# Optimization experiments

Hardware: AMD Instinct MI355X
Metric: run time of the kernel (lower is better)

Reference implementation:

```python
import jax, jax.numpy as jnp
import numpy as np

N = 100000
E = 1600000
F_NODE = 6
F_EDGE = 2
H = 64


def _glorot(key, shape):
    lim = float(np.sqrt(6.0 / (shape[0] + shape[1])))
    return jax.random.uniform(key, shape, jnp.float32, -lim, lim)


def setup_inputs() -> dict:
    key = jax.random.key(0)
    ks = jax.random.split(key, 16)
    inp = {
        "x": jax.random.normal(ks[0], (N, F_NODE), jnp.float32),
        "edge_index": jax.random.randint(ks[1], (2, E), 0, N, jnp.int64),
        "edge_attr": jax.random.normal(ks[2], (E, F_EDGE), jnp.float32),
        # GCN layers (PyG GCNConv: linear no-bias, then aggregate, then +bias)
        "W1": _glorot(ks[3], (F_NODE, H)), "b1": jnp.zeros((H,), jnp.float32),
        "W2": _glorot(ks[4], (H, H)), "b2": jnp.zeros((H,), jnp.float32),
        "W3": _glorot(ks[5], (H, H)), "b3": jnp.zeros((H,), jnp.float32),
        # edge_mlp
        "We1": _glorot(ks[6], (F_EDGE, H)), "be1": jnp.zeros((H,), jnp.float32),
        "We2": _glorot(ks[7], (H, H)), "be2": jnp.zeros((H,), jnp.float32),
        # predictor
        "Wp1": _glorot(ks[8], (3 * H, H)), "bp1": jnp.zeros((H,), jnp.float32),
        "Wp2": _glorot(ks[9], (H, H // 2)), "bp2": jnp.zeros((H // 2,), jnp.float32),
        "Wp3": _glorot(ks[10], (H // 2, 1)), "bp3": jnp.zeros((1,), jnp.float32),
    }
    return inp


def _gcn_conv(h, W, b, src_sl, dst_sl, norm, n):
    # PyG GCNConv with self-loops and symmetric normalization
    h = h @ W                                   # [N, H_out]
    msg = h[src_sl] * norm[:, None]             # gather + scale per edge(+loop)
    out = jax.ops.segment_sum(msg, dst_sl, num_segments=n)
    return out + b


def _forward(x, edge_attr, W1, b1, W2, b2, W3, b3, We1, be1, We2, be2,
             Wp1, bp1, Wp2, bp2, Wp3, bp3, edge_index):
    n = x.shape[0]
    src, dst = edge_index[0], edge_index[1]

    # --- edge feature injection (vectorized version of per-edge loop) ---
    ef = jax.nn.relu(edge_attr @ We1 + be1) @ We2 + be2      # [E, H]
    nef = (jax.ops.segment_sum(ef, src, num_segments=n)
           + jax.ops.segment_sum(ef, dst, num_segments=n))   # [N, H]
    ones_e = jnp.ones((ef.shape[0],), x.dtype)
    deg = (jax.ops.segment_sum(ones_e, src, num_segments=n)
           + jax.ops.segment_sum(ones_e, dst, num_segments=n))
    deg = jnp.maximum(deg, 1.0)
    nef = nef / deg[:, None]
    # hidden_dim (64) >= node feature dim (6) -> truncate
    x = x + nef[:, : x.shape[1]] * 0.5

    # --- GCN normalization with self-loops (shared across layers) ---
    loop = jnp.arange(n, dtype=src.dtype)
    src_sl = jnp.concatenate([src, loop])
    dst_sl = jnp.concatenate([dst, loop])
    deg_sl = jax.ops.segment_sum(jnp.ones_like(dst_sl, dtype=x.dtype), dst_sl,
                                 num_segments=n)
    dinv = jnp.where(deg_sl > 0, deg_sl ** -0.5, 0.0)
    norm = dinv[src_sl] * dinv[dst_sl]

    h = jax.nn.relu(_gcn_conv(x, W1, b1, src_sl, dst_sl, norm, n))
    h = jax.nn.relu(_gcn_conv(h, W2, b2, src_sl, dst_sl, norm, n))
    h = _gcn_conv(h, W3, b3, src_sl, dst_sl, norm, n)

    graph_emb = h.mean(axis=0)                 # global_mean_pool, batch=None
    node_mean = h.mean(axis=0)
    node_std = jnp.std(h, axis=0, ddof=1)      # torch.std is unbiased
    combined = jnp.concatenate([graph_emb, node_mean, node_std])  # [3H]

    p = jax.nn.relu(combined @ Wp1 + bp1)      # dropout inactive in eval
    p = jax.nn.relu(p @ Wp2 + bp2)
    out = jax.nn.sigmoid(p @ Wp3 + bp3)        # (1,)
    return out


def reference(x, edge_index, edge_attr, W1, b1, W2, b2, W3, b3,
              We1, be1, We2, be2, Wp1, bp1, Wp2, bp2, Wp3, bp3):
    return _forward(x, edge_attr, W1, b1, W2, b2, W3, b3, We1, be1, We2, be2,
                    Wp1, bp1, Wp2, bp2, Wp3, bp3, edge_index)
```

## Files before the change

### kernel.cpp

```cpp
#include <hip/hip_runtime.h>
#include <hip/hip_bf16.h>
#include <stdint.h>

typedef float floatx2 __attribute__((ext_vector_type(2)));
typedef unsigned uint32x4 __attribute__((ext_vector_type(4)));

__device__ __forceinline__ float rdlane(float v, int l) {
    return __uint_as_float(__builtin_amdgcn_readlane(__float_as_uint(v), l));
}
__device__ __forceinline__ unsigned pk_fp8x4(float a, float b, float c, float d) {
    int u = __builtin_amdgcn_cvt_pk_fp8_f32(a, b, 0, false);
    u = __builtin_amdgcn_cvt_pk_fp8_f32(c, d, u, true);
    return (unsigned)u;
}
__device__ __forceinline__ unsigned pk_fp8x2(float a, float b) {
    return (unsigned)__builtin_amdgcn_cvt_pk_fp8_f32(a, b, 0, false);
}

__global__ void k_zero(int* __restrict__ cntO, int* __restrict__ cntI,
                       double* __restrict__ sums, int n) {
    int i = blockIdx.x * blockDim.x + threadIdx.x;
    if (i < 128) sums[i] = 0.0;
    if (i < n) { cntO[i] = 0; cntI[i] = 0; }
}

__global__ __launch_bounds__(256) void k_front(
    const int* __restrict__ ei, const float* __restrict__ ea,
    const float* __restrict__ We1, const float* __restrict__ be1,
    const float* __restrict__ We2, const float* __restrict__ be2,
    uint2* __restrict__ efp, int* __restrict__ cntO, int* __restrict__ cntI,
    int* __restrict__ rankS, int* __restrict__ rankD, int E) {
    __shared__ float sWe1[128], sbe1[64], sWe2[64 * 6], sbe2[6];
    int t = threadIdx.x;
    if (t < 128) sWe1[t] = We1[t];
    if (t < 64) {
        sbe1[t] = be1[t];
#pragma unroll
        for (int c = 0; c < 6; ++c) sWe2[t * 6 + c] = We2[t * 64 + c];
    }
    if (t < 6) sbe2[t] = be2[t];
    __syncthreads();

    int e = blockIdx.x * blockDim.x + t;
    if (e >= E) return;

    int s = ei[e], d = ei[E + e];
    int rs = atomicAdd(&cntO[s], 1);
    int rd = atomicAdd(&cntI[d], 1);

    float2 aa = ((const float2*)ea)[e];
    float acc[6];
#pragma unroll
    for (int c = 0; c < 6; ++c) acc[c] = sbe2[c];
#pragma unroll
    for (int j = 0; j < 64; ++j) {
        float h = fmaf(aa.x, sWe1[j], fmaf(aa.y, sWe1[64 + j], sbe1[j]));
        h = fmaxf(h, 0.f);
#pragma unroll
        for (int c = 0; c < 6; ++c) acc[c] = fmaf(h, sWe2[j * 6 + c], acc[c]);
    }
    efp[e] = make_uint2(pk_fp8x4(acc[0], acc[1], acc[2], acc[3]),
                        pk_fp8x2(acc[4], acc[5]));
    rankS[e] = rs;
    rankD[e] = rd;
}

__global__ __launch_bounds__(256) void k_scan1(const int* __restrict__ cntO,
                                               const int* __restrict__ cntI,
                                               int2* __restrict__ bsum, int n) {
    __shared__ int2 l[256];
    int i = blockIdx.x * 256 + threadIdx.x;
    l[threadIdx.x] = (i < n) ? make_int2(cntO[i], cntI[i]) : make_int2(0, 0);
    __syncthreads();
    for (int s = 128; s > 0; s >>= 1) {
        if (threadIdx.x < s) {
            l[threadIdx.x].x += l[threadIdx.x + s].x;
            l[threadIdx.x].y += l[threadIdx.x + s].y;
        }
        __syncthreads();
    }
    if (threadIdx.x == 0) bsum[blockIdx.x] = l[0];
}
__global__ __launch_bounds__(512) void k_scan2(int2* __restrict__ bsum, int nb,
                                               int* __restrict__ offON,
                                               int* __restrict__ offIN) {
    __shared__ int2 l[512];
    int t = threadIdx.x;
    int2 v = (t < nb) ? bsum[t] : make_int2(0, 0);
    l[t] = v;
    __syncthreads();
    for (int s = 1; s < 512; s <<= 1) {
        int2 tmp = (t >= s) ? l[t - s] : make_int2(0, 0);
        __syncthreads();
        l[t].x += tmp.x; l[t].y += tmp.y;
        __syncthreads();
    }
    if (t < nb) bsum[t] = make_int2(l[t].x - v.x, l[t].y - v.y);
    if (t == 511) { *offON = l[511].x; *offIN = l[511].y; }
}
__global__ __launch_bounds__(256) void k_scan3off(const int* __restrict__ cntO,
                                                  const int* __restrict__ cntI,
                                                  const int2* __restrict__ bsum,
                                                  int* __restrict__ offO,
                                                  int* __restrict__ offI, int n) {
    __shared__ int2 l[256];
    int i = blockIdx.x * 256 + threadIdx.x;
    int2 v = (i < n) ? make_int2(cntO[i], cntI[i]) : make_int2(0, 0);
    l[threadIdx.x] = v;
    __syncthreads();
    for (int s = 1; s < 256; s <<= 1) {
        int2 tmp = (threadIdx.x >= (unsigned)s) ? l[threadIdx.x - s] : make_int2(0, 0);
        __syncthreads();
        l[threadIdx.x].x += tmp.x; l[threadIdx.x].y += tmp.y;
        __syncthreads();
    }
    if (i < n) {
        int2 bs = bsum[blockIdx.x];
        offO[i] = l[threadIdx.x].x - v.x + bs.x;
        offI[i] = l[threadIdx.x].y - v.y + bs.y;
    }
}

__global__ __launch_bounds__(256) void k_place(const int* __restrict__ ei,
                                               const int* __restrict__ rankS,
                                               const int* __restrict__ rankD,
                                               const int* __restrict__ offO,
                                               const int* __restrict__ offI,
                                               const uint2* __restrict__ efp,
                                               uint2* __restrict__ out_rec,
                                               uint4* __restrict__ in_rec, int E) {
    int e = blockIdx.x * blockDim.x + threadIdx.x;
    if (e >= E) return;
    int s = ei[e], d = ei[E + e];
    uint2 f = efp[e];
    out_rec[offO[s] + rankS[e]] = f;
    in_rec[offI[d] + rankD[e]] = make_uint4((unsigned)s, f.x, f.y, 0u);
}

__global__ __launch_bounds__(256) void k_nefmm1(
    const int* __restrict__ offO, const uint2* __restrict__ out_rec,
    const int* __restrict__ offI, const uint4* __restrict__ in_rec,
    const float* __restrict__ x, const float* __restrict__ W1,
    float* __restrict__ dinv, int* __restrict__ in_src,
    unsigned* __restrict__ sOut, int n) {
    __shared__ float sW1[384];
    int t = threadIdx.x;
    for (int idx = t; idx < 384; idx += 256) sW1[idx] = W1[idx];
    __syncthreads();

    int i = blockIdx.x * blockDim.x + t;
    if (i >= n) return;
    int bo = offO[i], eo = offO[i + 1];
    int bi = offI[i], eiN = offI[i + 1];
    float a0 = 0.f, a1 = 0.f, a2 = 0.f, a3 = 0.f, a4 = 0.f, a5 = 0.f;
    for (int j = bo; j < eo; ++j) {
        uint2 q = out_rec[j];
        floatx2 p01 = __builtin_amdgcn_cvt_pk_f32_fp8(q.x, false);
        floatx2 p23 = __builtin_amdgcn_cvt_pk_f32_fp8(q.x, true);
        floatx2 p45 = __builtin_amdgcn_cvt_pk_f32_fp8(q.y, false);
        a0 += p01.x; a1 += p01.y; a2 += p23.x;
        a3 += p23.y; a4 += p45.x; a5 += p45.y;
    }
    for (int j = bi; j < eiN; ++j) {
        uint4 r = in_rec[j];
        __builtin_nontemporal_store((int)r.x, in_src + j);
        floatx2 p01 = __builtin_amdgcn_cvt_pk_f32_fp8(r.y, false);
        floatx2 p23 = __builtin_amdgcn_cvt_pk_f32_fp8(r.y, true);
        floatx2 p45 = __builtin_amdgcn_cvt_pk_f32_fp8(r.z, false);
        a0 += p01.x; a1 += p01.y; a2 += p23.x;
        a3 += p23.y; a4 += p45.x; a5 += p45.y;
    }
    int indeg = eiN - bi;
    float degf = (float)((eo - bo) + indeg);
    float inv = 0.5f / fmaxf(degf, 1.f);
    const float2* xr = (const float2*)(x + (size_t)i * 6);
    float2 x01 = xr[0], x23 = xr[1], x45 = xr[2];
    float xp0 = x01.x + a0 * inv, xp1 = x01.y + a1 * inv;
    float xp2 = x23.x + a2 * inv, xp3 = x23.y + a3 * inv;
    float xp4 = x45.x + a4 * inv, xp5 = x45.y + a5 * inv;
    float dv = 1.f / sqrtf(1.f + (float)indeg);
    dinv[i] = dv;

    unsigned u[16];
#pragma unroll
    for (int c4 = 0; c4 < 16; ++c4) {
        float tv[4];
#pragma unroll
        for (int k = 0; k < 4; ++k) {
            int c = c4 * 4 + k;
            float v = xp0 * sW1[c] + xp1 * sW1[64 + c] + xp2 * sW1[128 + c]
                    + xp3 * sW1[192 + c] + xp4 * sW1[256 + c] + xp5 * sW1[320 + c];
            tv[k] = v * dv;
        }
        u[c4] = pk_fp8x4(tv[0], tv[1], tv[2], tv[3]);
    }
#pragma unroll
    for (int q4 = 0; q4 < 4; ++q4) {
        uint32x4 v = {u[q4 * 4 + 0], u[q4 * 4 + 1], u[q4 * 4 + 2], u[q4 * 4 + 3]};
        __builtin_nontemporal_store(v, (uint32x4*)(sOut + (size_t)i * 16) + q4);
    }
}

__global__ __launch_bounds__(256) void k_gathermm(
    const int* __restrict__ offI, const int* __restrict__ in_src,
    const float* __restrict__ dinv, const unsigned* __restrict__ sIn,
    const float* __restrict__ bias, const float* __restrict__ W,
    unsigned* __restrict__ sOut, int n) {
    int lane = threadIdx.x & 63;
    int sub = lane & 15, grp = lane >> 4;
    int wid = (blockIdx.x * blockDim.x + threadIdx.x) >> 6;
    int nw = (gridDim.x * blockDim.x) >> 6;
    float w[64];
#pragma unroll
    for (int c = 0; c < 64; ++c) w[c] = W[c * 64 + lane];
    float4 bb = ((const float4*)bias)[sub];

    for (int i = wid; i < n; i += nw) {
        unsigned su = sIn[(size_t)i * 16 + sub];
        float a0, a1, a2, a3;
        if (grp == 0) {
            floatx2 lo = __builtin_amdgcn_cvt_pk_f32_fp8(su, false);
            floatx2 hi = __builtin_amdgcn_cvt_pk_f32_fp8(su, true);
            a0 = lo.x; a1 = lo.y; a2 = hi.x; a3 = hi.y;
        } else { a0 = a1 = a2 = a3 = 0.f; }
        int b0 = offI[i], e0 = offI[i + 1];
#pragma unroll 4
        for (int j = b0 + grp; j < e0; j += 4) {
            unsigned src = (unsigned)__builtin_nontemporal_load(in_src + j);
            unsigned u = sIn[(size_t)src * 16 + sub];
            floatx2 lo = __builtin_amdgcn_cvt_pk_f32_fp8(u, false);
            floatx2 hi = __builtin_amdgcn_cvt_pk_f32_fp8(u, true);
            a0 += lo.x; a1 += lo.y; a2 += hi.x; a3 += hi.y;
        }
        a0 += __shfl_xor(a0, 16); a1 += __shfl_xor(a1, 16);
        a2 += __shfl_xor(a2, 16); a3 += __shfl_xor(a3, 16);
        a0 += __shfl_xor(a0, 32); a1 += __shfl_xor(a1, 32);
        a2 += __shfl_xor(a2, 32); a3 += __shfl_xor(a3, 32);

        float dv = dinv[i];
        float h0 = fmaxf(fmaf(a0, dv, bb.x), 0.f);
        float h1 = fmaxf(fmaf(a1, dv, bb.y), 0.f);
        float h2 = fmaxf(fmaf(a2, dv, bb.z), 0.f);
        float h3 = fmaxf(fmaf(a3, dv, bb.w), 0.f);
        float o = 0.f;
#pragma unroll
        for (int g = 0; g < 16; ++g) {
            o = fmaf(rdlane(h0, g), w[g * 4 + 0], o);
            o = fmaf(rdlane(h1, g), w[g * 4 + 1], o);
            o = fmaf(rdlane(h2, g), w[g * 4 + 2], o);
            o = fmaf(rdlane(h3, g), w[g * 4 + 3], o);
        }
        o *= dv;
        float o0 = __shfl(o, sub * 4 + 0);
        float o1 = __shfl(o, sub * 4 + 1);
        float o2 = __shfl(o, sub * 4 + 2);
        float o3 = __shfl(o, sub * 4 + 3);
        if (lane < 16)
            __builtin_nontemporal_store(pk_fp8x4(o0, o1, o2, o3),
                                        sOut + (size_t)i * 16 + lane);
    }
}

__global__ __launch_bounds__(256) void k_gatherreduce(
    const int* __restrict__ offI, const int* __restrict__ in_src,
    const float* __restrict__ dinv, const unsigned* __restrict__ sIn,
    const float* __restrict__ b3, double* __restrict__ sums, int n) {
    int lane = threadIdx.x & 63;
    int sub = lane & 15, grp = lane >> 4;
    int wv = threadIdx.x >> 6;
    int wid = (blockIdx.x * blockDim.x + threadIdx.x) >> 6;
    int nw = (gridDim.x * blockDim.x) >> 6;
    float4 bb = ((const float4*)b3)[sub];
    double s0 = 0.0, s1 = 0.0, s2_ = 0.0, s3 = 0.0;
    double q0 = 0.0, q1 = 0.0, q2 = 0.0, q3 = 0.0;

    for (int i = wid; i < n; i += nw) {
        unsigned su = sIn[(size_t)i * 16 + sub];
        float a0, a1, a2, a3;
        if (grp == 0) {
            floatx2 lo = __builtin_amdgcn_cvt_pk_f32_fp8(su, false);
            floatx2 hi = __builtin_amdgcn_cvt_pk_f32_fp8(su, true);
            a0 = lo.x; a1 = lo.y; a2 = hi.x; a3 = hi.y;
        } else { a0 = a1 = a2 = a3 = 0.f; }
        int b0 = offI[i], e0 = offI[i + 1];
#pragma unroll 4
        for (int j = b0 + grp; j < e0; j += 4) {
            unsigned src = (unsigned)__builtin_nontemporal_load(in_src + j);
            unsigned u = sIn[(size_t)src * 16 + sub];
            floatx2 lo = __builtin_amdgcn_cvt_pk_f32_fp8(u, false);
            floatx2 hi = __builtin_amdgcn_cvt_pk_f32_fp8(u, true);
            a0 += lo.x; a1 += lo.y; a2 += hi.x; a3 += hi.y;
        }
        a0 += __shfl_xor(a0, 16); a1 += __shfl_xor(a1, 16);
        a2 += __shfl_xor(a2, 16); a3 += __shfl_xor(a3, 16);
        a0 += __shfl_xor(a0, 32); a1 += __shfl_xor(a1, 32);
        a2 += __shfl_xor(a2, 32); a3 += __shfl_xor(a3, 32);

        float dv = dinv[i];
        float v0 = fmaf(a0, dv, bb.x);
        float v1 = fmaf(a1, dv, bb.y);
        float v2 = fmaf(a2, dv, bb.z);
        float v3 = fmaf(a3, dv, bb.w);
        s0 += v0; s1 += v1; s2_ += v2; s3 += v3;
        q0 += (double)v0 * v0; q1 += (double)v1 * v1;
        q2 += (double)v2 * v2; q3 += (double)v3 * v3;
    }
    __shared__ double shS[4 * 64], shQ[4 * 64];
    if (grp == 0) {
#pragma unroll
        for (int k = 0; k < 4; ++k) {
            double sk = (k == 0) ? s0 : (k == 1) ? s1 : (k == 2) ? s2_ : s3;
            double qk = (k == 0) ? q0 : (k == 1) ? q1 : (k == 2) ? q2 : q3;
            shS[wv * 64 + sub * 4 + k] = sk;
            shQ[wv * 64 + sub * 4 + k] = qk;
        }
    }
    __syncthreads();
    if (wv == 0) {
        double a = shS[lane] + shS[64 + lane] + shS[128 + lane] + shS[192 + lane];
        double c = shQ[lane] + shQ[64 + lane] + shQ[128 + lane] + shQ[192 + lane];
        unsafeAtomicAdd(&sums[lane], a);
        unsafeAtomicAdd(&sums[64 + lane], c);
    }
}

__global__ void k_head(const double* __restrict__ sums,
                       const float* __restrict__ Wp1, const float* __restrict__ bp1,
                       const float* __restrict__ Wp2, const float* __restrict__ bp2,
                       const float* __restrict__ Wp3, const float* __restrict__ bp3,
                       float* __restrict__ out, int n) {
    __shared__ float comb[192], p1[64], p2[32];
    int t = threadIdx.x;
    if (t < 64) {
        double s = sums[t], s2 = sums[64 + t];
        double m = s / n;
        double var = (s2 - s * s / n) / (double)(n - 1);
        float mf = (float)m;
        float sd = (float)sqrt(var > 0.0 ? var : 0.0);
        comb[t] = mf;
        comb[64 + t] = mf;
        comb[128 + t] = sd;
    }
    __syncthreads();
    if (t < 64) {
        float acc = bp1[t];
        for (int k = 0; k < 192; ++k) acc = fmaf(comb[k], Wp1[k * 64 + t], acc);
        p1[t] = fmaxf(acc, 0.f);
    }
    __syncthreads();
    if (t < 32) {
        float acc = bp2[t];
        for (int k = 0; k < 64; ++k) acc = fmaf(p1[k], Wp2[k * 32 + t], acc);
        p2[t] = fmaxf(acc, 0.f);
    }
    __syncthreads();
    if (t == 0) {
        float acc = bp3[0];
        for (int k = 0; k < 32; ++k) acc = fmaf(p2[k], Wp3[k], acc);
        out[0] = 1.f / (1.f + expf(-acc));
    }
}

static inline char* align16(char* p) {
    return (char*)(((uintptr_t)p + 15) & ~(uintptr_t)15);
}

extern "C" void kernel_launch(void* const* d_in, const int* in_sizes, int n_in,
                              void* d_out, int out_size, void* d_ws, size_t ws_size,
                              hipStream_t stream) {
    const float* x   = (const float*)d_in[0];
    const int*   ei  = (const int*)d_in[1];
    const float* ea  = (const float*)d_in[2];
    const float* W1  = (const float*)d_in[3];
    const float* b1  = (const float*)d_in[4];
    const float* W2  = (const float*)d_in[5];
    const float* b2  = (const float*)d_in[6];
    const float* W3  = (const float*)d_in[7];
    const float* b3  = (const float*)d_in[8];
    const float* We1 = (const float*)d_in[9];
    const float* be1 = (const float*)d_in[10];
    const float* We2 = (const float*)d_in[11];
    const float* be2 = (const float*)d_in[12];
    const float* Wp1 = (const float*)d_in[13];
    const float* bp1 = (const float*)d_in[14];
    const float* Wp2 = (const float*)d_in[15];
    const float* bp2 = (const float*)d_in[16];
    const float* Wp3 = (const float*)d_in[17];
    const float* bp3 = (const float*)d_in[18];

    const int N = in_sizes[0] / 6;
    const int E = in_sizes[1] / 2;
    const int nbN = (N + 255) / 256;
    const int nbE = (E + 255) / 256;
    const size_t SB = ((size_t)N * 64 + 15) & ~(size_t)15;

    char* p = (char*)d_ws;
    double* sums = (double*)p;          p = align16(p + 128 * sizeof(double));
    int* cntO = (int*)p;                p = align16(p + (size_t)N * 4);
    int* cntI = (int*)p;                p = align16(p + (size_t)N * 4);
    int* offO = (int*)p;                p = align16(p + ((size_t)N + 1) * 4);
    int* offI = (int*)p;                p = align16(p + ((size_t)N + 1) * 4);
    int2* bsum = (int2*)p;              p = align16(p + 512 * 8);
    float* dinv = (float*)p;            p = align16(p + (size_t)N * 4);
    int* in_src = (int*)p;              p = align16(p + (size_t)E * 4);
    uint4* in_rec = (uint4*)p;          p = align16(p + (size_t)E * 16);
    char* u1 = p;                       p = align16(p + 2 * SB);
    int* rankS = (int*)u1;
    int* rankD = (int*)(u1 + SB);
    unsigned* sbufA = (unsigned*)u1;
    unsigned* sbufB = (unsigned*)(u1 + SB);
    char* u2 = p;
    uint2* efp = (uint2*)u2;
    uint2* out_rec = (uint2*)(u2 + (size_t)E * 8);

    dim3 blk(256);

    k_zero<<<dim3(nbN), blk, 0, stream>>>(cntO, cntI, sums, N);
    k_front<<<dim3(nbE), blk, 0, stream>>>(ei, ea, We1, be1, We2, be2,
                                           efp, cntO, cntI, rankS, rankD, E);
    k_scan1<<<dim3(nbN), blk, 0, stream>>>(cntO, cntI, bsum, N);
    k_scan2<<<dim3(1), dim3(512), 0, stream>>>(bsum, nbN, offO + N, offI + N);
    k_scan3off<<<dim3(nbN), blk, 0, stream>>>(cntO, cntI, bsum, offO, offI, N);
    k_place<<<dim3(nbE), blk, 0, stream>>>(ei, rankS, rankD, offO, offI, efp,
                                           out_rec, in_rec, E);
    k_nefmm1<<<dim3(nbN), blk, 0, stream>>>(offO, out_rec, offI, in_rec, x, W1,
                                            dinv, in_src, sbufA, N);

    k_gathermm<<<dim3(2048), blk, 0, stream>>>(offI, in_src, dinv, sbufA, b1, W2, sbufB, N);
    k_gathermm<<<dim3(2048), blk, 0, stream>>>(offI, in_src, dinv, sbufB, b2, W3, sbufA, N);
    k_gatherreduce<<<dim3(2048), blk, 0, stream>>>(offI, in_src, dinv, sbufA, b3, sums, N);
    k_head<<<dim3(1), dim3(64), 0, stream>>>(sums, Wp1, bp1, Wp2, bp2, Wp3, bp3,
                                             (float*)d_out, N);
}
```

Before: 603.0 us.

## Partition degree-count atomics into eight per-block-group copies to cut contention

Splits the per-node out/in edge counters into eight partitions selected by block index, so the counting atomics in the front kernel spread across more addresses. A new column-scan kernel turns the partitioned counts into per-partition bases and per-node totals, and the placement kernel adds the partition base when computing CSR positions. This adds zeroing and scanning of eight times larger count arrays, an extra kernel launch, and extra scattered reads in placement. Random endpoints already see little contention, so the gain may be small.

New measurement: 628.6 us. 4.2% more time.

```diff
diff --git a/kernel.cpp b/kernel.cpp
--- a/kernel.cpp
+++ b/kernel.cpp
@@ -17,19 +17,19 @@
     return (unsigned)__builtin_amdgcn_cvt_pk_fp8_f32(a, b, 0, false);
 }
 
-__global__ void k_zero(int* __restrict__ cntO, int* __restrict__ cntI,
-                       double* __restrict__ sums, int n) {
+__global__ void k_zero(int* __restrict__ cntO8, int* __restrict__ cntI8,
+                       double* __restrict__ sums, int n8) {
     int i = blockIdx.x * blockDim.x + threadIdx.x;
     if (i < 128) sums[i] = 0.0;
-    if (i < n) { cntO[i] = 0; cntI[i] = 0; }
+    if (i < n8) { cntO8[i] = 0; cntI8[i] = 0; }
 }
 
 __global__ __launch_bounds__(256) void k_front(
     const int* __restrict__ ei, const float* __restrict__ ea,
     const float* __restrict__ We1, const float* __restrict__ be1,
     const float* __restrict__ We2, const float* __restrict__ be2,
-    uint2* __restrict__ efp, int* __restrict__ cntO, int* __restrict__ cntI,
-    int* __restrict__ rankS, int* __restrict__ rankD, int E) {
+    uint2* __restrict__ efp, int* __restrict__ cntO8, int* __restrict__ cntI8,
+    int* __restrict__ rankS, int* __restrict__ rankD, int E, int N) {
     __shared__ float sWe1[128], sbe1[64], sWe2[64 * 6], sbe2[6];
     int t = threadIdx.x;
     if (t < 128) sWe1[t] = We1[t];
@@ -43,10 +43,11 @@
 
     int e = blockIdx.x * blockDim.x + t;
     if (e >= E) return;
+    int part = blockIdx.x & 7;
 
     int s = ei[e], d = ei[E + e];
-    int rs = atomicAdd(&cntO[s], 1);
-    int rd = atomicAdd(&cntI[d], 1);
+    int rs = atomicAdd(&cntO8[(size_t)part * N + s], 1);
+    int rd = atomicAdd(&cntI8[(size_t)part * N + d], 1);
 
     float2 aa = ((const float2*)ea)[e];
     float acc[6];
@@ -63,6 +64,30 @@
                         pk_fp8x2(acc[4], acc[5]));
     rankS[e] = rs;
     rankD[e] = rd;
+}
+
+__global__ __launch_bounds__(256) void k_colscan(int* __restrict__ cntO8,
+                                                 int* __restrict__ cntI8,
+                                                 int* __restrict__ totO,
+                                                 int* __restrict__ totI, int n) {
+    int i = blockIdx.x * blockDim.x + threadIdx.x;
+    if (i >= n) return;
+    int run = 0;
+#pragma unroll
+    for (int p = 0; p < 8; ++p) {
+        int v = cntO8[(size_t)p * n + i];
+        cntO8[(size_t)p * n + i] = run;
+        run += v;
+    }
+    totO[i] = run;
+    run = 0;
+#pragma unroll
+    for (int p = 0; p < 8; ++p) {
+        int v = cntI8[(size_t)p * n + i];
+        cntI8[(size_t)p * n + i] = run;
+        run += v;
+    }
+    totI[i] = run;
 }
 
 __global__ __launch_bounds__(256) void k_scan1(const int* __restrict__ cntO,
@@ -126,15 +151,20 @@
                                                const int* __restrict__ rankD,
                                                const int* __restrict__ offO,
                                                const int* __restrict__ offI,
+                                               const int* __restrict__ baseO8,
+                                               const int* __restrict__ baseI8,
                                                const uint2* __restrict__ efp,
                                                uint2* __restrict__ out_rec,
-                                               uint4* __restrict__ in_rec, int E) {
+                                               uint4* __restrict__ in_rec,
+                                               int E, int N) {
     int e = blockIdx.x * blockDim.x + threadIdx.x;
     if (e >= E) return;
+    int part = blockIdx.x & 7;
     int s = ei[e], d = ei[E + e];
     uint2 f = efp[e];
-    out_rec[offO[s] + rankS[e]] = f;
-    in_rec[offI[d] + rankD[e]] = make_uint4((unsigned)s, f.x, f.y, 0u);
+    out_rec[offO[s] + baseO8[(size_t)part * N + s] + rankS[e]] = f;
+    in_rec[offI[d] + baseI8[(size_t)part * N + d] + rankD[e]] =
+        make_uint4((unsigned)s, f.x, f.y, 0u);
 }
 
 __global__ __launch_bounds__(256) void k_nefmm1(
@@ -392,12 +422,15 @@
     const int E = in_sizes[1] / 2;
     const int nbN = (N + 255) / 256;
     const int nbE = (E + 255) / 256;
+    const int N8 = 8 * N;
     const size_t SB = ((size_t)N * 64 + 15) & ~(size_t)15;
 
     char* p = (char*)d_ws;
     double* sums = (double*)p;          p = align16(p + 128 * sizeof(double));
-    int* cntO = (int*)p;                p = align16(p + (size_t)N * 4);
-    int* cntI = (int*)p;                p = align16(p + (size_t)N * 4);
+    int* cntO8 = (int*)p;               p = align16(p + (size_t)N8 * 4);
+    int* cntI8 = (int*)p;               p = align16(p + (size_t)N8 * 4);
+    int* totO = (int*)p;                p = align16(p + (size_t)N * 4);
+    int* totI = (int*)p;                p = align16(p + (size_t)N * 4);
     int* offO = (int*)p;                p = align16(p + ((size_t)N + 1) * 4);
     int* offI = (int*)p;                p = align16(p + ((size_t)N + 1) * 4);
     int2* bsum = (int2*)p;              p = align16(p + 512 * 8);
@@ -415,14 +448,15 @@
 
     dim3 blk(256);
 
-    k_zero<<<dim3(nbN), blk, 0, stream>>>(cntO, cntI, sums, N);
+    k_zero<<<dim3((N8 + 255) / 256), blk, 0, stream>>>(cntO8, cntI8, sums, N8);
     k_front<<<dim3(nbE), blk, 0, stream>>>(ei, ea, We1, be1, We2, be2,
-                                           efp, cntO, cntI, rankS, rankD, E);
-    k_scan1<<<dim3(nbN), blk, 0, stream>>>(cntO, cntI, bsum, N);
+                                           efp, cntO8, cntI8, rankS, rankD, E, N);
+    k_colscan<<<dim3(nbN), blk, 0, stream>>>(cntO8, cntI8, totO, totI, N);
+    k_scan1<<<dim3(nbN), blk, 0, stream>>>(totO, totI, bsum, N);
     k_scan2<<<dim3(1), dim3(512), 0, stream>>>(bsum, nbN, offO + N, offI + N);
-    k_scan3off<<<dim3(nbN), blk, 0, stream>>>(cntO, cntI, bsum, offO, offI, N);
-    k_place<<<dim3(nbE), blk, 0, stream>>>(ei, rankS, rankD, offO, offI, efp,
-                                           out_rec, in_rec, E);
+    k_scan3off<<<dim3(nbN), blk, 0, stream>>>(totO, totI, bsum, offO, offI, N);
+    k_place<<<dim3(nbE), blk, 0, stream>>>(ei, rankS, rankD, offO, offI,
+                                           cntO8, cntI8, efp, out_rec, in_rec, E, N);
     k_nefmm1<<<dim3(nbN), blk, 0, stream>>>(offO, out_rec, offI, in_rec, x, W1,
                                             dinv, in_src, sbufA, N);
 
```
